# Kernel optimization log

Measured on AMD Instinct MI355X. Metric: run time of the kernel, lower is better.

Reference implementation:

```python
import jax, jax.numpy as jnp
import numpy as np

DEPTH, HEADS, DIM_HEAD, DIM, MLP, PATCH_DIM, NP_, NC = 8, 8, 64, 512, 2048, 512, 1024, 2
INNER = HEADS * DIM_HEAD
SCALE = DIM_HEAD ** -0.5
EPS = 1e-5

def layernorm(x, s, b):
    m = x.mean(-1, keepdims=True)
    v = ((x - m) ** 2).mean(-1, keepdims=True)
    return (x - m) * jax.lax.rsqrt(v + EPS) * s + b

def setup_inputs() -> dict:
    key = jax.random.key(0)
    ks = jax.random.split(key, 24)
    g = lambda k, sh, sc=0.02: jax.random.normal(k, sh, dtype=jnp.float32) * sc
    return {
        "img": jax.random.normal(ks[0], (4, NP_, PATCH_DIM), dtype=jnp.float32),
        "embed_w": g(ks[1], (PATCH_DIM, DIM)), "embed_b": jnp.zeros((DIM,), jnp.float32),
        "pos_emb": g(ks[2], (1, NP_ + 1, DIM), 1.0), "cls_token": g(ks[3], (1, 1, DIM), 1.0),
        "ln1_s": jnp.ones((DEPTH, DIM), jnp.float32), "ln1_b": jnp.zeros((DEPTH, DIM), jnp.float32),
        "qkv_w": g(ks[4], (DEPTH, DIM, 3 * INNER)),
        "out_w": g(ks[5], (DEPTH, INNER, DIM)), "out_b": jnp.zeros((DEPTH, DIM), jnp.float32),
        "ln2_s": jnp.ones((DEPTH, DIM), jnp.float32), "ln2_b": jnp.zeros((DEPTH, DIM), jnp.float32),
        "ff_w1": g(ks[6], (DEPTH, DIM, MLP)), "ff_b1": jnp.zeros((DEPTH, MLP), jnp.float32),
        "ff_w2": g(ks[7], (DEPTH, MLP, DIM)), "ff_b2": jnp.zeros((DEPTH, DIM), jnp.float32),
        "head_ln_s": jnp.ones((DIM,), jnp.float32), "head_ln_b": jnp.zeros((DIM,), jnp.float32),
        "head_w": g(ks[8], (DIM, NC)), "head_b": jnp.zeros((NC,), jnp.float32),
    }

def reference(img, embed_w, embed_b, pos_emb, cls_token, ln1_s, ln1_b, qkv_w, out_w, out_b,
              ln2_s, ln2_b, ff_w1, ff_b1, ff_w2, ff_b2, head_ln_s, head_ln_b, head_w, head_b):
    B, N, _ = img.shape
    x = img @ embed_w + embed_b                       # [B, N, DIM]
    cls = jnp.broadcast_to(cls_token, (B, 1, DIM))
    x = jnp.concatenate([cls, x], axis=1) + pos_emb[:, :N + 1]
    for l in range(DEPTH):
        h = layernorm(x, ln1_s[l], ln1_b[l])
        qkv = h @ qkv_w[l]                            # [B, N+1, 3*INNER]
        q, k, v = jnp.split(qkv, 3, axis=-1)
        rh = lambda t: t.reshape(B, N + 1, HEADS, DIM_HEAD).transpose(0, 2, 1, 3)
        q, k, v = rh(q), rh(k), rh(v)                 # [B, H, N+1, Dh]
        dots = jnp.einsum('bhnd,bhmd->bhnm', q, k) * SCALE
        attn = jax.nn.softmax(dots, axis=-1)
        o = jnp.einsum('bhnm,bhmd->bhnd', attn, v)
        o = o.transpose(0, 2, 1, 3).reshape(B, N + 1, INNER)
        x = o @ out_w[l] + out_b[l] + x
        h = layernorm(x, ln2_s[l], ln2_b[l])
        h = jax.nn.gelu(h @ ff_w1[l] + ff_b1[l], approximate=False)
        x = h @ ff_w2[l] + ff_b2[l] + x
    x = x[:, 0]                                       # cls pooling
    x = layernorm(x, head_ln_s, head_ln_b)
    return (jax.nn.sigmoid(x @ head_w + head_b),)
```

## Files before the change

### kernel.cpp

```cpp
#include <hip/hip_runtime.h>
#include <math.h>
#include <stdint.h>

#define NHEADS   8
#define DHEAD    64
#define DIMM     512
#define MLPD     2048
#define NPATCH   1024
#define NTOK     1025
#define BATCH    4
#define ROWS     (BATCH*NTOK)
#define TOKPAD   1088
#define NCHUNK   17
#define CSPLIT   9
#define QSC      0.180336881f
#define LN_EPS   1e-5f

typedef __attribute__((ext_vector_type(8))) short short8;
typedef __attribute__((ext_vector_type(4))) float f32x4;

__device__ __forceinline__ unsigned short f2bf(float f) {
  union { float f; unsigned u; } c; c.f = f;
  unsigned u = c.u;
  return (unsigned short)((u + 0x7fffu + ((u >> 16) & 1u)) >> 16);
}
__device__ __forceinline__ unsigned short f2bf_fast(float f) {
  union { float f; unsigned u; } c; c.f = f;
  return (unsigned short)((c.u + 0x8000u) >> 16);
}
__device__ __forceinline__ float bf2f(unsigned short b) {
  union { unsigned u; float f; } c; c.u = (unsigned)b << 16;
  return c.f;
}

__device__ __forceinline__ float wsum(float v) {
#pragma unroll
  for (int o = 32; o > 0; o >>= 1) v += __shfl_xor(v, o, 64);
  return v;
}

__device__ __forceinline__ void gl_lds16(const void* g, const void* l) {
  __builtin_amdgcn_global_load_lds(
      (const __attribute__((address_space(1))) unsigned int*)(uintptr_t)g,
      (__attribute__((address_space(3))) unsigned int*)(unsigned int)(uintptr_t)l,
      16, 0, 0);
}

template <int TM, int TN, int WR, int WC, bool ACOMB>
__global__ __launch_bounds__(256) void mgemm_k(
    const unsigned short* __restrict__ A, const unsigned short* __restrict__ Bt,
    const float* __restrict__ bias, const float* __restrict__ res,
    void* __restrict__ Cout, int M, int N, int K, int flags,
    unsigned short* __restrict__ vTout, const float* __restrict__ mlc)
{
  constexpr int AF = TM / WR / 16;
  constexpr int BF = TN / WC / 16;
  constexpr int AG = TM / 32;
  constexpr int BG = TN / 32;
  __shared__ unsigned short sA[2][TM * 64];
  __shared__ unsigned short sB[2][TN * 64];
  const int tid = threadIdx.x;
  const int w = tid >> 6, lane = tid & 63;
  const int quad = lane >> 4, l15 = lane & 15;
  const int m0 = blockIdx.y * TM, n0 = blockIdx.x * TN;
  const int wrow = (w / WC) * (TM / WR);
  const int wcol = (w % WC) * (TN / WC);
  const int lrow = lane >> 3;
  const int lkg = (lane & 7) ^ lrow;

  size_t abase[AG], bbase[BG];
  int arow[AG];
#pragma unroll
  for (int g = 0; g < AG; g++) {
    int grp = w * AG + g;
    int ar = m0 + grp * 8 + lrow; ar = ar < M ? ar : M - 1;
    arow[g] = ar;
    abase[g] = (size_t)ar * K + lkg * 8;
  }
#pragma unroll
  for (int g = 0; g < BG; g++) {
    int grp = w * BG + g;
    int br = n0 + grp * 8 + lrow;
    bbase[g] = (size_t)br * K + lkg * 8;
  }

  auto stageB = [&](int k0, int buf) {
#pragma unroll
    for (int g = 0; g < BG; g++)
      gl_lds16(Bt + bbase[g] + k0, &sB[buf][(w * BG + g) * 512]);
  };
  auto stageA_dma = [&](int k0, int buf) {
#pragma unroll
    for (int g = 0; g < AG; g++)
      gl_lds16(A + abase[g] + k0, &sA[buf][(w * AG + g) * 512]);
  };

  uint4 ra0[AG], ra1[AG];
  float rl0[AG], rl1[AG];
  auto loadA = [&](int k0) {
    const int h = k0 >> 6;
#pragma unroll
    for (int g = 0; g < AG; g++) {
      size_t off = abase[g] + k0;
      ra0[g] = *(const uint4*)(A + off);
      ra1[g] = *(const uint4*)(A + (size_t)ROWS * DIMM + off);
      int b = arow[g] / NTOK, tok = arow[g] - b * NTOK;
      int bh = b * 8 + h;
      rl0[g] = mlc[(size_t)bh * NTOK + tok];
      rl1[g] = mlc[(size_t)(32 + bh) * NTOK + tok];
    }
  };
  auto writeA = [&](int buf) {
#pragma unroll
    for (int g = 0; g < AG; g++) {
      float inv = 1.0f / (rl0[g] + rl1[g]);
      const unsigned short* p0 = (const unsigned short*)&ra0[g];
      const unsigned short* p1 = (const unsigned short*)&ra1[g];
      alignas(16) unsigned short o[8];
#pragma unroll
      for (int i = 0; i < 8; i++)
        o[i] = f2bf((bf2f(p0[i]) + bf2f(p1[i])) * inv);
      *(uint4*)&sA[buf][(w * AG + g) * 512 + lane * 8] = *(const uint4*)o;
    }
  };

  f32x4 acc[AF][BF];
#pragma unroll
  for (int i = 0; i < AF; i++)
#pragma unroll
    for (int j = 0; j < BF; j++) { f32x4 z = {0.f, 0.f, 0.f, 0.f}; acc[i][j] = z; }

  if (ACOMB) { stageB(0, 0); loadA(0); writeA(0); }
  else       { stageA_dma(0, 0); stageB(0, 0); }

  const int nsteps = K >> 6;
  for (int step = 0; step < nsteps; step++) {
    const int buf = step & 1;
    __syncthreads();
    if (step + 1 < nsteps) {
      stageB((step + 1) << 6, buf ^ 1);
      if (ACOMB) loadA((step + 1) << 6);
      else       stageA_dma((step + 1) << 6, buf ^ 1);
    }
#pragma unroll
    for (int kk = 0; kk < 2; kk++) {
      short8 af[AF], bfr[BF];
#pragma unroll
      for (int i = 0; i < AF; i++) {
        int r = wrow + i * 16 + l15;
        af[i] = *(const short8*)&sA[buf][r * 64 + (((kk * 4 + quad) ^ (lane & 7)) << 3)];
      }
#pragma unroll
      for (int j = 0; j < BF; j++) {
        int r = wcol + j * 16 + l15;
        bfr[j] = *(const short8*)&sB[buf][r * 64 + (((kk * 4 + quad) ^ (lane & 7)) << 3)];
      }
#pragma unroll
      for (int i = 0; i < AF; i++)
#pragma unroll
        for (int j = 0; j < BF; j++)
          acc[i][j] = __builtin_amdgcn_mfma_f32_16x16x32_bf16(af[i], bfr[j], acc[i][j], 0, 0, 0);
    }
    if (ACOMB && step + 1 < nsteps) writeA(buf ^ 1);
  }

  const bool do_gelu = flags & 1;
  const bool out_bf  = flags & 2;
#pragma unroll
  for (int i = 0; i < AF; i++) {
#pragma unroll
    for (int j = 0; j < BF; j++) {
      const int col = n0 + wcol + j * 16 + l15;
      const bool vcol = (vTout != nullptr) && (col >= 1024);
      alignas(8) unsigned short vb[4];
#pragma unroll
      for (int rg = 0; rg < 4; rg++) {
        int row = m0 + wrow + i * 16 + quad * 4 + rg;
        if (row >= M) continue;
        float v = acc[i][j][rg];
        if (bias) v += bias[col];
        if (do_gelu) v = 0.5f * v * (1.0f + erff(v * 0.70710678118654752f));
        if (res) v += res[(size_t)row * N + col];
        if (out_bf) {
          unsigned short bv = f2bf(v);
          vb[rg] = bv;
          if (!vcol) ((unsigned short*)Cout)[(size_t)row * N + col] = bv;
        } else {
          ((float*)Cout)[(size_t)row * N + col] = v;
        }
      }
      if (vcol) {
        const int hcol = col - 1024, h = hcol >> 6, d = hcol & 63;
#pragma unroll
        for (int rg = 0; rg < 4; rg++) {
          int row = m0 + wrow + i * 16 + quad * 4 + rg;
          if (row >= M) continue;
          int bb = row / NTOK, tok = row - bb * NTOK;
          vTout[((size_t)(bb * 8 + h) * 64 + d) * TOKPAD + tok] = vb[rg];
        }
      }
    }
  }
}

__global__ __launch_bounds__(256) void attn_k(
    const unsigned short* __restrict__ qkv, const unsigned short* __restrict__ vT,
    unsigned short* __restrict__ po, float* __restrict__ ml)
{
  __shared__ unsigned short ps[64 * 64];
  __shared__ unsigned short ks[2][64 * 64];
  __shared__ unsigned short vs[2][64 * 64];
  const int bh = blockIdx.x, b = bh >> 3, h = bh & 7;
  const int q0 = blockIdx.y * 64;
  const int split = blockIdx.z;
  const int tid = threadIdx.x, w = tid >> 6, lane = tid & 63;
  const int quad = lane >> 4, l15 = lane & 15;
  const int lrow = lane >> 3, lkg = (lane & 7) ^ lrow;
  const unsigned short* qbase = qkv + (size_t)(b * NTOK) * 1536 + h * 64;
  const unsigned short* kbase = qbase + 512;
  const unsigned short* vtb   = vT + (size_t)bh * 64 * TOKPAD;

  auto stage_kv = [&](int c0, int buf) {
#pragma unroll
    for (int g = 0; g < 2; g++) {
      int grp = w * 2 + g;
      int tok = c0 + grp * 8 + lrow; tok = tok < NTOK ? tok : NTOK - 1;
      gl_lds16(kbase + (size_t)tok * 1536 + lkg * 8, &ks[buf][grp * 512]);
      int d = grp * 8 + lrow;
      gl_lds16(vtb + (size_t)d * TOKPAD + c0 + lkg * 8, &vs[buf][grp * 512]);
    }
  };

  const int cbeg = split ? CSPLIT : 0;
  const int cend = split ? NCHUNK : CSPLIT;
  stage_kv(cbeg * 64, 0);

  int qr = q0 + w * 16 + l15; qr = qr < NTOK ? qr : NTOK - 1;
  const unsigned short* qrow = qbase + (size_t)qr * 1536;
  short8 aq[2];
  aq[0] = *(const short8*)(qrow + quad * 8);
  aq[1] = *(const short8*)(qrow + 32 + quad * 8);
#pragma unroll
  for (int k = 0; k < 2; k++)
#pragma unroll
    for (int i = 0; i < 8; i++)
      aq[k][i] = (short)f2bf(bf2f((unsigned short)aq[k][i]) * QSC);

  short8 ones;
#pragma unroll
  for (int i = 0; i < 8; i++) ones[i] = (short)0x3F80;

  f32x4 Oa[4];
#pragma unroll
  for (int n = 0; n < 4; n++) { f32x4 z = {0.f, 0.f, 0.f, 0.f}; Oa[n] = z; }
  float lst[4] = {0.f, 0.f, 0.f, 0.f};

  for (int c = cbeg; c < cend; c++) {
    const int c0 = c * 64;
    const int buf = (c - cbeg) & 1;
    __syncthreads();
    if (c + 1 < cend) stage_kv(c0 + 64, buf ^ 1);

    f32x4 sa[4];
#pragma unroll
    for (int n = 0; n < 4; n++) {
      f32x4 s = {0.f, 0.f, 0.f, 0.f};
#pragma unroll
      for (int kk = 0; kk < 2; kk++) {
        short8 bk = *(const short8*)&ks[buf][(n * 16 + l15) * 64 + (((kk * 4 + quad) ^ (lane & 7)) << 3)];
        s = __builtin_amdgcn_mfma_f32_16x16x32_bf16(aq[kk], bk, s, 0, 0, 0);
      }
      sa[n] = s;
    }

    if (c0 + 64 > NTOK) {
#pragma unroll
      for (int n = 0; n < 4; n++) {
        bool oob = (c0 + n * 16 + l15) >= NTOK;
#pragma unroll
        for (int rg = 0; rg < 4; rg++)
          if (oob) sa[n][rg] = -1e30f;
      }
    }

#pragma unroll
    for (int n = 0; n < 4; n++)
#pragma unroll
      for (int rg = 0; rg < 4; rg++) {
        int row = w * 16 + quad * 4 + rg;
        int key = n * 16 + l15;
        ps[row * 64 + ((((key >> 3) ^ (row & 7)) & 7) << 3) + (key & 7)] =
            f2bf_fast(exp2f(sa[n][rg]));
      }

    short8 ap[2];
#pragma unroll
    for (int kk = 0; kk < 2; kk++)
      ap[kk] = *(const short8*)&ps[(w * 16 + l15) * 64 + (((kk * 4 + quad) ^ (lane & 7)) << 3)];

    f32x4 lsum = {0.f, 0.f, 0.f, 0.f};
#pragma unroll
    for (int kk = 0; kk < 2; kk++)
      lsum = __builtin_amdgcn_mfma_f32_16x16x32_bf16(ap[kk], ones, lsum, 0, 0, 0);
#pragma unroll
    for (int rg = 0; rg < 4; rg++) lst[rg] += lsum[rg];

#pragma unroll
    for (int n = 0; n < 4; n++) {
      f32x4 o = Oa[n];
#pragma unroll
      for (int kk = 0; kk < 2; kk++) {
        short8 bv = *(const short8*)&vs[buf][(n * 16 + l15) * 64 + (((kk * 4 + quad) ^ (lane & 7)) << 3)];
        o = __builtin_amdgcn_mfma_f32_16x16x32_bf16(ap[kk], bv, o, 0, 0, 0);
      }
      Oa[n] = o;
    }
  }

  unsigned short* pob = po + (size_t)split * ROWS * DIMM;
#pragma unroll
  for (int n = 0; n < 4; n++)
#pragma unroll
    for (int rg = 0; rg < 4; rg++) {
      int tok = q0 + w * 16 + quad * 4 + rg;
      if (tok < NTOK)
        pob[(size_t)(b * NTOK + tok) * DIMM + h * 64 + n * 16 + l15] = f2bf(Oa[n][rg]);
    }
  if (l15 == 0) {
#pragma unroll
    for (int rg = 0; rg < 4; rg++) {
      int tok = q0 + w * 16 + quad * 4 + rg;
      if (tok < NTOK)
        ml[(size_t)(split * 32 + bh) * NTOK + tok] = lst[rg];
    }
  }
}

__global__ __launch_bounds__(256) void ln_k(
    const float* __restrict__ X, const float* __restrict__ s,
    const float* __restrict__ b, unsigned short* __restrict__ Y, int nrows)
{
  const int w = threadIdx.x >> 6, lane = threadIdx.x & 63;
  const int row = blockIdx.x * 4 + w;
  if (row >= nrows) return;
  const float* x = X + (size_t)row * DIMM;
  float4 v0 = *(const float4*)(x + lane * 8);
  float4 v1 = *(const float4*)(x + lane * 8 + 4);
  float xv[8] = {v0.x, v0.y, v0.z, v0.w, v1.x, v1.y, v1.z, v1.w};
  float sum = 0.f, sq = 0.f;
#pragma unroll
  for (int i = 0; i < 8; i++) { sum += xv[i]; sq += xv[i] * xv[i]; }
  sum = wsum(sum); sq = wsum(sq);
  const float mean = sum * (1.0f / DIMM);
  const float var  = sq * (1.0f / DIMM) - mean * mean;
  const float r    = rsqrtf(var + LN_EPS);
  alignas(16) unsigned short tmp[8];
#pragma unroll
  for (int i = 0; i < 8; i++) {
    int d = lane * 8 + i;
    tmp[i] = f2bf((xv[i] - mean) * r * s[d] + b[d]);
  }
  *(uint4*)&Y[(size_t)row * DIMM + lane * 8] = *(const uint4*)tmp;
}

__global__ __launch_bounds__(256) void assemble_k(
    const float* __restrict__ emb, const float* __restrict__ cls,
    const float* __restrict__ pos, float* __restrict__ X)
{
  int idx = blockIdx.x * 256 + threadIdx.x;
  if (idx >= BATCH * NTOK * DIMM) return;
  int d = idx & (DIMM - 1);
  int t = (idx >> 9) % NTOK;
  int b = idx / (NTOK * DIMM);
  float v = (t == 0) ? cls[d] : emb[((size_t)b * NPATCH + (t - 1)) * DIMM + d];
  X[idx] = v + pos[(size_t)t * DIMM + d];
}

__global__ __launch_bounds__(256) void cast_k(
    const float* __restrict__ X, unsigned short* __restrict__ Y, int n4)
{
  int i = blockIdx.x * 256 + threadIdx.x;
  if (i >= n4) return;
  float4 v = ((const float4*)X)[i];
  alignas(8) unsigned short o[4] = {f2bf(v.x), f2bf(v.y), f2bf(v.z), f2bf(v.w)};
  ((uint2*)Y)[i] = *(const uint2*)o;
}

__global__ __launch_bounds__(256) void tcast_k(
    const float* __restrict__ W, unsigned short* __restrict__ Wt, int K, int N)
{
  __shared__ float t[32][33];
  const size_t off = (size_t)blockIdx.z * K * N;
  W += off; Wt += off;
  int n0 = blockIdx.x * 32, k0 = blockIdx.y * 32;
  int tx = threadIdx.x & 31, ty = threadIdx.x >> 5;
#pragma unroll
  for (int i = 0; i < 4; i++)
    t[ty + 8 * i][tx] = W[(size_t)(k0 + ty + 8 * i) * N + n0 + tx];
  __syncthreads();
#pragma unroll
  for (int i = 0; i < 4; i++) {
    int n = ty + 8 * i;
    Wt[(size_t)(n0 + n) * K + k0 + tx] = f2bf(t[tx][n]);
  }
}

__global__ __launch_bounds__(256) void head_k(
    const float* __restrict__ X, const float* __restrict__ s,
    const float* __restrict__ bln, const float* __restrict__ W,
    const float* __restrict__ bh, float* __restrict__ out)
{
  const int w = threadIdx.x >> 6, lane = threadIdx.x & 63;
  if (w >= BATCH) return;
  const float* x = X + (size_t)w * NTOK * DIMM;
  float4 v0 = *(const float4*)(x + lane * 8);
  float4 v1 = *(const float4*)(x + lane * 8 + 4);
  float xv[8] = {v0.x, v0.y, v0.z, v0.w, v1.x, v1.y, v1.z, v1.w};
  float sum = 0.f, sq = 0.f;
#pragma unroll
  for (int i = 0; i < 8; i++) { sum += xv[i]; sq += xv[i] * xv[i]; }
  sum = wsum(sum); sq = wsum(sq);
  const float mean = sum * (1.0f / DIMM);
  const float var  = sq * (1.0f / DIMM) - mean * mean;
  const float r    = rsqrtf(var + LN_EPS);
  float l0 = 0.f, l1 = 0.f;
#pragma unroll
  for (int i = 0; i < 8; i++) {
    int d = lane * 8 + i;
    float xn = (xv[i] - mean) * r * s[d] + bln[d];
    l0 = fmaf(xn, W[d * 2 + 0], l0);
    l1 = fmaf(xn, W[d * 2 + 1], l1);
  }
  l0 = wsum(l0); l1 = wsum(l1);
  if (lane == 0) {
    out[w * 2 + 0] = 1.0f / (1.0f + expf(-(l0 + bh[0])));
    out[w * 2 + 1] = 1.0f / (1.0f + expf(-(l1 + bh[1])));
  }
}

extern "C" void kernel_launch(void* const* d_in, const int* in_sizes, int n_in,
                              void* d_out, int out_size, void* d_ws, size_t ws_size,
                              hipStream_t stream)
{
  const float* img       = (const float*)d_in[0];
  const float* embed_w   = (const float*)d_in[1];
  const float* embed_b   = (const float*)d_in[2];
  const float* pos_emb   = (const float*)d_in[3];
  const float* cls_token = (const float*)d_in[4];
  const float* ln1_s     = (const float*)d_in[5];
  const float* ln1_b     = (const float*)d_in[6];
  const float* qkv_w     = (const float*)d_in[7];
  const float* out_w     = (const float*)d_in[8];
  const float* out_b     = (const float*)d_in[9];
  const float* ln2_s     = (const float*)d_in[10];
  const float* ln2_b     = (const float*)d_in[11];
  const float* ff_w1     = (const float*)d_in[12];
  const float* ff_b1     = (const float*)d_in[13];
  const float* ff_w2     = (const float*)d_in[14];
  const float* ff_b2     = (const float*)d_in[15];
  const float* head_ln_s = (const float*)d_in[16];
  const float* head_ln_b = (const float*)d_in[17];
  const float* head_w    = (const float*)d_in[18];
  const float* head_b    = (const float*)d_in[19];
  float* out = (float*)d_out;

  char* p = (char*)d_ws;
  auto alloc = [&](size_t bytes) { char* r = p; p += (bytes + 255) & ~(size_t)255; return r; };

  unsigned short* wt_embed = (unsigned short*)alloc((size_t)512 * 512 * 2);
  unsigned short* wt_qkv   = (unsigned short*)alloc((size_t)8 * 1536 * 512 * 2);
  unsigned short* wt_out   = (unsigned short*)alloc((size_t)8 * 512 * 512 * 2);
  unsigned short* wt_ff1   = (unsigned short*)alloc((size_t)8 * 2048 * 512 * 2);
  unsigned short* wt_ff2   = (unsigned short*)alloc((size_t)8 * 512 * 2048 * 2);
  unsigned short* img_bf   = (unsigned short*)alloc((size_t)4096 * 512 * 2);
  float*          x        = (float*)alloc((size_t)ROWS * DIMM * 4);
  unsigned short* h        = (unsigned short*)alloc((size_t)ROWS * DIMM * 2);
  unsigned short* vTb      = (unsigned short*)alloc((size_t)32 * 64 * TOKPAD * 2);
  unsigned short* po       = (unsigned short*)alloc((size_t)2 * ROWS * DIMM * 2);
  float*          mlb      = (float*)alloc((size_t)2 * 32 * NTOK * 4);
  char*           big      = alloc((size_t)ROWS * MLPD * 2);
  unsigned short* qkvb     = (unsigned short*)big;
  unsigned short* ffh      = (unsigned short*)big;
  float*          embuf    = (float*)big;

  dim3 blk(256);

  cast_k<<<(4096 * 512 / 4 + 255) / 256, blk, 0, stream>>>(img, img_bf, 4096 * 512 / 4);
  tcast_k<<<dim3(16, 16, 1), blk, 0, stream>>>(embed_w, wt_embed, 512, 512);
  tcast_k<<<dim3(48, 16, 8), blk, 0, stream>>>(qkv_w, wt_qkv, 512, 1536);
  tcast_k<<<dim3(16, 16, 8), blk, 0, stream>>>(out_w, wt_out, 512, 512);
  tcast_k<<<dim3(64, 16, 8), blk, 0, stream>>>(ff_w1, wt_ff1, 512, 2048);
  tcast_k<<<dim3(16, 64, 8), blk, 0, stream>>>(ff_w2, wt_ff2, 2048, 512);

  mgemm_k<64, 64, 2, 2, false><<<dim3(8, 64), blk, 0, stream>>>(
      img_bf, wt_embed, embed_b, nullptr, embuf, 4096, 512, 512, 0, nullptr, nullptr);
  assemble_k<<<(BATCH * NTOK * DIMM + 255) / 256, blk, 0, stream>>>(
      embuf, cls_token, pos_emb, x);

  const int mt64 = (ROWS + 63) / 64;
  for (int l = 0; l < 8; l++) {
    ln_k<<<(ROWS + 3) / 4, blk, 0, stream>>>(
        x, ln1_s + l * DIMM, ln1_b + l * DIMM, h, ROWS);
    mgemm_k<64, 128, 1, 4, false><<<dim3(12, mt64), blk, 0, stream>>>(
        h, wt_qkv + (size_t)l * 1536 * 512, nullptr, nullptr,
        qkvb, ROWS, 1536, 512, 2, vTb, nullptr);
    attn_k<<<dim3(32, 17, 2), blk, 0, stream>>>(qkvb, vTb, po, mlb);
    mgemm_k<64, 64, 2, 2, true><<<dim3(8, mt64), blk, 0, stream>>>(
        po, wt_out + (size_t)l * 512 * 512, out_b + l * DIMM, x,
        x, ROWS, 512, 512, 0, nullptr, mlb);
    ln_k<<<(ROWS + 3) / 4, blk, 0, stream>>>(
        x, ln2_s + l * DIMM, ln2_b + l * DIMM, h, ROWS);
    mgemm_k<64, 128, 1, 4, false><<<dim3(16, mt64), blk, 0, stream>>>(
        h, wt_ff1 + (size_t)l * 2048 * 512, ff_b1 + l * MLPD, nullptr,
        ffh, ROWS, 2048, 512, 1 | 2, nullptr, nullptr);
    mgemm_k<64, 64, 2, 2, false><<<dim3(8, mt64), blk, 0, stream>>>(
        ffh, wt_ff2 + (size_t)l * 512 * 2048, ff_b2 + l * DIMM, x,
        x, ROWS, 512, 2048, 0, nullptr, nullptr);
  }

  head_k<<<1, blk, 0, stream>>>(x, head_ln_s, head_ln_b, head_w, head_b, out);
}
```

Before: 1.304 ms.

## Fuse LayerNorm into GEMM A-loading using per-row stats from residual epilogues

Removes the standalone LayerNorm kernels. The residual-add GEMM epilogues (out-proj, FF2, and assemble) now write per-column-block partial sums and sums of squares per row. The QKV and FF1 GEMMs then reduce those partials into mean and rstd and normalise fp32 x on the fly while staging A into LDS. This saves two kernel launches per layer and the bf16 h round trip, at the cost of register-path A loads in place of DMA-to-LDS, a redundant fp32 read of x by every column tile, and a single-pass variance formula.

```diff
diff --git a/kernel.cpp b/kernel.cpp
--- a/kernel.cpp
+++ b/kernel.cpp
@@ -46,12 +46,14 @@
       16, 0, 0);
 }
 
-template <int TM, int TN, int WR, int WC, bool ACOMB>
+template <int TM, int TN, int WR, int WC, int MODE>
 __global__ __launch_bounds__(256) void mgemm_k(
     const unsigned short* __restrict__ A, const unsigned short* __restrict__ Bt,
     const float* __restrict__ bias, const float* __restrict__ res,
     void* __restrict__ Cout, int M, int N, int K, int flags,
-    unsigned short* __restrict__ vTout, const float* __restrict__ mlc)
+    unsigned short* __restrict__ vTout, const float* __restrict__ mlc,
+    const float* __restrict__ xsrc, const float* __restrict__ lns,
+    const float* __restrict__ lnb, float* __restrict__ statout)
 {
   constexpr int AF = TM / WR / 16;
   constexpr int BF = TN / WC / 16;
@@ -97,7 +99,7 @@
 
   uint4 ra0[AG], ra1[AG];
   float rl0[AG], rl1[AG];
-  auto loadA = [&](int k0) {
+  auto loadAC = [&](int k0) {
     const int h = k0 >> 6;
 #pragma unroll
     for (int g = 0; g < AG; g++) {
@@ -110,7 +112,7 @@
       rl1[g] = mlc[(size_t)(32 + bh) * NTOK + tok];
     }
   };
-  auto writeA = [&](int buf) {
+  auto writeAC = [&](int buf) {
 #pragma unroll
     for (int g = 0; g < AG; g++) {
       float inv = 1.0f / (rl0[g] + rl1[g]);
@@ -124,14 +126,63 @@
     }
   };
 
+  float amean[AG], arstd[AG];
+  float4 xs0[AG], xs1[AG], sv0, sv1, bv0, bv1;
+  if (MODE == 2) {
+#pragma unroll
+    for (int g = 0; g < AG; g++) {
+      const float4* pr = (const float4*)(mlc + (size_t)arow[g] * 32);
+      float s = 0.f, q = 0.f;
+#pragma unroll
+      for (int t = 0; t < 8; t++) {
+        float4 v = pr[t];
+        s += v.x + v.z; q += v.y + v.w;
+      }
+      float mean = s * (1.0f / DIMM);
+      float var  = q * (1.0f / DIMM) - mean * mean;
+      amean[g] = mean;
+      arstd[g] = rsqrtf(var + LN_EPS);
+    }
+  }
+  auto loadLN = [&](int k0) {
+    sv0 = *(const float4*)(lns + k0 + lkg * 8);
+    sv1 = *(const float4*)(lns + k0 + lkg * 8 + 4);
+    bv0 = *(const float4*)(lnb + k0 + lkg * 8);
+    bv1 = *(const float4*)(lnb + k0 + lkg * 8 + 4);
+#pragma unroll
+    for (int g = 0; g < AG; g++) {
+      const float* xr = xsrc + (size_t)arow[g] * DIMM + k0 + lkg * 8;
+      xs0[g] = *(const float4*)xr;
+      xs1[g] = *(const float4*)(xr + 4);
+    }
+  };
+  auto writeLN = [&](int buf) {
+#pragma unroll
+    for (int g = 0; g < AG; g++) {
+      const float m = amean[g], r = arstd[g];
+      alignas(16) unsigned short o[8];
+      o[0] = f2bf((xs0[g].x - m) * r * sv0.x + bv0.x);
+      o[1] = f2bf((xs0[g].y - m) * r * sv0.y + bv0.y);
+      o[2] = f2bf((xs0[g].z - m) * r * sv0.z + bv0.z);
+      o[3] = f2bf((xs0[g].w - m) * r * sv0.w + bv0.w);
+      o[4] = f2bf((xs1[g].x - m) * r * sv1.x + bv1.x);
+      o[5] = f2bf((xs1[g].y - m) * r * sv1.y + bv1.y);
+      o[6] = f2bf((xs1[g].z - m) * r * sv1.z + bv1.z);
+      o[7] = f2bf((xs1[g].w - m) * r * sv1.w + bv1.w);
+      *(uint4*)&sA[buf][(w * AG + g) * 512 + lane * 8] = *(const uint4*)o;
+    }
+  };
+
   f32x4 acc[AF][BF];
 #pragma unroll
   for (int i = 0; i < AF; i++)
 #pragma unroll
     for (int j = 0; j < BF; j++) { f32x4 z = {0.f, 0.f, 0.f, 0.f}; acc[i][j] = z; }
 
-  if (ACOMB) { stageB(0, 0); loadA(0); writeA(0); }
-  else       { stageA_dma(0, 0); stageB(0, 0); }
+  stageB(0, 0);
+  if (MODE == 0)      { stageA_dma(0, 0); }
+  else if (MODE == 1) { loadAC(0); writeAC(0); }
+  else                { loadLN(0); writeLN(0); }
 
   const int nsteps = K >> 6;
   for (int step = 0; step < nsteps; step++) {
@@ -139,8 +190,9 @@
     __syncthreads();
     if (step + 1 < nsteps) {
       stageB((step + 1) << 6, buf ^ 1);
-      if (ACOMB) loadA((step + 1) << 6);
-      else       stageA_dma((step + 1) << 6, buf ^ 1);
+      if (MODE == 0)      stageA_dma((step + 1) << 6, buf ^ 1);
+      else if (MODE == 1) loadAC((step + 1) << 6);
+      else                loadLN((step + 1) << 6);
     }
 #pragma unroll
     for (int kk = 0; kk < 2; kk++) {
@@ -161,11 +213,20 @@
         for (int j = 0; j < BF; j++)
           acc[i][j] = __builtin_amdgcn_mfma_f32_16x16x32_bf16(af[i], bfr[j], acc[i][j], 0, 0, 0);
     }
-    if (ACOMB && step + 1 < nsteps) writeA(buf ^ 1);
+    if (step + 1 < nsteps) {
+      if (MODE == 1)      writeAC(buf ^ 1);
+      else if (MODE == 2) writeLN(buf ^ 1);
+    }
   }
 
   const bool do_gelu = flags & 1;
   const bool out_bf  = flags & 2;
+  float psum[AF][4], psq[AF][4];
+#pragma unroll
+  for (int i = 0; i < AF; i++)
+#pragma unroll
+    for (int rg = 0; rg < 4; rg++) { psum[i][rg] = 0.f; psq[i][rg] = 0.f; }
+
 #pragma unroll
   for (int i = 0; i < AF; i++) {
 #pragma unroll
@@ -181,6 +242,7 @@
         if (bias) v += bias[col];
         if (do_gelu) v = 0.5f * v * (1.0f + erff(v * 0.70710678118654752f));
         if (res) v += res[(size_t)row * N + col];
+        if (statout) { psum[i][rg] += v; psq[i][rg] += v * v; }
         if (out_bf) {
           unsigned short bv = f2bf(v);
           vb[rg] = bv;
@@ -200,6 +262,28 @@
         }
       }
     }
+  }
+
+  if (statout) {
+    const int cb = blockIdx.x * (TN / 32) + (w % WC);
+#pragma unroll
+    for (int i = 0; i < AF; i++)
+#pragma unroll
+      for (int rg = 0; rg < 4; rg++) {
+        float s = psum[i][rg], q = psq[i][rg];
+#pragma unroll
+        for (int o = 8; o > 0; o >>= 1) {
+          s += __shfl_xor(s, o, 64);
+          q += __shfl_xor(q, o, 64);
+        }
+        if (l15 == 0) {
+          int row = m0 + wrow + i * 16 + quad * 4 + rg;
+          if (row < M) {
+            statout[(size_t)row * 32 + cb * 2 + 0] = s;
+            statout[(size_t)row * 32 + cb * 2 + 1] = q;
+          }
+        }
+      }
   }
 }
 
@@ -336,44 +420,32 @@
   }
 }
 
-__global__ __launch_bounds__(256) void ln_k(
-    const float* __restrict__ X, const float* __restrict__ s,
-    const float* __restrict__ b, unsigned short* __restrict__ Y, int nrows)
+__global__ __launch_bounds__(256) void assemble_k(
+    const float* __restrict__ emb, const float* __restrict__ cls,
+    const float* __restrict__ pos, float* __restrict__ X,
+    float* __restrict__ statout)
 {
   const int w = threadIdx.x >> 6, lane = threadIdx.x & 63;
   const int row = blockIdx.x * 4 + w;
-  if (row >= nrows) return;
-  const float* x = X + (size_t)row * DIMM;
-  float4 v0 = *(const float4*)(x + lane * 8);
-  float4 v1 = *(const float4*)(x + lane * 8 + 4);
-  float xv[8] = {v0.x, v0.y, v0.z, v0.w, v1.x, v1.y, v1.z, v1.w};
+  if (row >= ROWS) return;
+  const int b = row / NTOK, t = row - b * NTOK;
+  const int d0 = lane * 8;
+  const float* src = (t == 0) ? cls : emb + ((size_t)b * NPATCH + (t - 1)) * DIMM;
+  float4 a0 = *(const float4*)(src + d0);
+  float4 a1 = *(const float4*)(src + d0 + 4);
+  float4 p0 = *(const float4*)(pos + (size_t)t * DIMM + d0);
+  float4 p1 = *(const float4*)(pos + (size_t)t * DIMM + d0 + 4);
+  float v[8] = {a0.x + p0.x, a0.y + p0.y, a0.z + p0.z, a0.w + p0.w,
+                a1.x + p1.x, a1.y + p1.y, a1.z + p1.z, a1.w + p1.w};
+  float* xr = X + (size_t)row * DIMM + d0;
+  *(float4*)xr       = make_float4(v[0], v[1], v[2], v[3]);
+  *(float4*)(xr + 4) = make_float4(v[4], v[5], v[6], v[7]);
   float sum = 0.f, sq = 0.f;
 #pragma unroll
-  for (int i = 0; i < 8; i++) { sum += xv[i]; sq += xv[i] * xv[i]; }
+  for (int i = 0; i < 8; i++) { sum += v[i]; sq += v[i] * v[i]; }
   sum = wsum(sum); sq = wsum(sq);
-  const float mean = sum * (1.0f / DIMM);
-  const float var  = sq * (1.0f / DIMM) - mean * mean;
-  const float r    = rsqrtf(var + LN_EPS);
-  alignas(16) unsigned short tmp[8];
-#pragma unroll
-  for (int i = 0; i < 8; i++) {
-    int d = lane * 8 + i;
-    tmp[i] = f2bf((xv[i] - mean) * r * s[d] + b[d]);
-  }
-  *(uint4*)&Y[(size_t)row * DIMM + lane * 8] = *(const uint4*)tmp;
-}
-
-__global__ __launch_bounds__(256) void assemble_k(
-    const float* __restrict__ emb, const float* __restrict__ cls,
-    const float* __restrict__ pos, float* __restrict__ X)
-{
-  int idx = blockIdx.x * 256 + threadIdx.x;
-  if (idx >= BATCH * NTOK * DIMM) return;
-  int d = idx & (DIMM - 1);
-  int t = (idx >> 9) % NTOK;
-  int b = idx / (NTOK * DIMM);
-  float v = (t == 0) ? cls[d] : emb[((size_t)b * NPATCH + (t - 1)) * DIMM + d];
-  X[idx] = v + pos[(size_t)t * DIMM + d];
+  if (lane < 32)
+    statout[(size_t)row * 32 + lane] = lane == 0 ? sum : (lane == 1 ? sq : 0.f);
 }
 
 __global__ __launch_bounds__(256) void cast_k(
@@ -474,10 +546,11 @@
   unsigned short* wt_ff2   = (unsigned short*)alloc((size_t)8 * 512 * 2048 * 2);
   unsigned short* img_bf   = (unsigned short*)alloc((size_t)4096 * 512 * 2);
   float*          x        = (float*)alloc((size_t)ROWS * DIMM * 4);
-  unsigned short* h        = (unsigned short*)alloc((size_t)ROWS * DIMM * 2);
   unsigned short* vTb      = (unsigned short*)alloc((size_t)32 * 64 * TOKPAD * 2);
   unsigned short* po       = (unsigned short*)alloc((size_t)2 * ROWS * DIMM * 2);
   float*          mlb      = (float*)alloc((size_t)2 * 32 * NTOK * 4);
+  float*          st1      = (float*)alloc((size_t)ROWS * 32 * 4);
+  float*          st2      = (float*)alloc((size_t)ROWS * 32 * 4);
   char*           big      = alloc((size_t)ROWS * MLPD * 2);
   unsigned short* qkvb     = (unsigned short*)big;
   unsigned short* ffh      = (unsigned short*)big;
@@ -492,30 +565,29 @@
   tcast_k<<<dim3(64, 16, 8), blk, 0, stream>>>(ff_w1, wt_ff1, 512, 2048);
   tcast_k<<<dim3(16, 64, 8), blk, 0, stream>>>(ff_w2, wt_ff2, 2048, 512);
 
-  mgemm_k<64, 64, 2, 2, false><<<dim3(8, 64), blk, 0, stream>>>(
-      img_bf, wt_embed, embed_b, nullptr, embuf, 4096, 512, 512, 0, nullptr, nullptr);
-  assemble_k<<<(BATCH * NTOK * DIMM + 255) / 256, blk, 0, stream>>>(
-      embuf, cls_token, pos_emb, x);
+  mgemm_k<64, 64, 2, 2, 0><<<dim3(8, 64), blk, 0, stream>>>(
+      img_bf, wt_embed, embed_b, nullptr, embuf, 4096, 512, 512, 0,
+      nullptr, nullptr, nullptr, nullptr, nullptr, nullptr);
+  assemble_k<<<(ROWS + 3) / 4, blk, 0, stream>>>(
+      embuf, cls_token, pos_emb, x, st1);
 
   const int mt64 = (ROWS + 63) / 64;
   for (int l = 0; l < 8; l++) {
-    ln_k<<<(ROWS + 3) / 4, blk, 0, stream>>>(
-        x, ln1_s + l * DIMM, ln1_b + l * DIMM, h, ROWS);
-    mgemm_k<64, 128, 1, 4, false><<<dim3(12, mt64), blk, 0, stream>>>(
-        h, wt_qkv + (size_t)l * 1536 * 512, nullptr, nullptr,
-        qkvb, ROWS, 1536, 512, 2, vTb, nullptr);
+    mgemm_k<64, 128, 1, 4, 2><<<dim3(12, mt64), blk, 0, stream>>>(
+        nullptr, wt_qkv + (size_t)l * 1536 * 512, nullptr, nullptr,
+        qkvb, ROWS, 1536, 512, 2, vTb, st1, x,
+        ln1_s + l * DIMM, ln1_b + l * DIMM, nullptr);
     attn_k<<<dim3(32, 17, 2), blk, 0, stream>>>(qkvb, vTb, po, mlb);
-    mgemm_k<64, 64, 2, 2, true><<<dim3(8, mt64), blk, 0, stream>>>(
+    mgemm_k<64, 64, 2, 2, 1><<<dim3(8, mt64), blk, 0, stream>>>(
         po, wt_out + (size_t)l * 512 * 512, out_b + l * DIMM, x,
-        x, ROWS, 512, 512, 0, nullptr, mlb);
-    ln_k<<<(ROWS + 3) / 4, blk, 0, stream>>>(
-        x, ln2_s + l * DIMM, ln2_b + l * DIMM, h, ROWS);
-    mgemm_k<64, 128, 1, 4, false><<<dim3(16, mt64), blk, 0, stream>>>(
-        h, wt_ff1 + (size_t)l * 2048 * 512, ff_b1 + l * MLPD, nullptr,
-        ffh, ROWS, 2048, 512, 1 | 2, nullptr, nullptr);
-    mgemm_k<64, 64, 2, 2, false><<<dim3(8, mt64), blk, 0, stream>>>(
+        x, ROWS, 512, 512, 0, nullptr, mlb, nullptr, nullptr, nullptr, st2);
+    mgemm_k<64, 128, 1, 4, 2><<<dim3(16, mt64), blk, 0, stream>>>(
+        nullptr, wt_ff1 + (size_t)l * 2048 * 512, ff_b1 + l * MLPD, nullptr,
+        ffh, ROWS, 2048, 512, 1 | 2, nullptr, st2, x,
+        ln2_s + l * DIMM, ln2_b + l * DIMM, nullptr);
+    mgemm_k<64, 64, 2, 2, 0><<<dim3(8, mt64), blk, 0, stream>>>(
         ffh, wt_ff2 + (size_t)l * 512 * 2048, ff_b2 + l * DIMM, x,
-        x, ROWS, 512, 2048, 0, nullptr, nullptr);
+        x, ROWS, 512, 2048, 0, nullptr, nullptr, nullptr, nullptr, nullptr, st1);
   }
 
   head_k<<<1, blk, 0, stream>>>(x, head_ln_s, head_ln_b, head_w, head_b, out);
```

After: 1.406 ms. 7.8% more time.
